# Performance work log

Measured on AMD Instinct MI355X. Metric: run time of the kernel, lower is better.

The kernel has to match this reference:

```python
import jax, jax.numpy as jnp
import numpy as np

# subgraph partition for subgraph_num == 7 (sums to 78 nodes)
GRAPH_LIST = [5, 9, 9, 25, 9, 9, 12]
EMB_SIZE = 30
PROJ_DIM = 10


def setup_inputs() -> dict:
    key = jax.random.key(0)
    k_x, k_c, k_w = jax.random.split(key, 3)
    B, N = 32768, sum(GRAPH_LIST)  # N = 78
    x = jax.random.normal(k_x, (B, N, EMB_SIZE), dtype=jnp.float32)
    coordinates = jax.random.normal(k_c, (N, 3), dtype=jnp.float32)
    stdv = 1.0 / np.sqrt(62.0)  # matches reset_parameters (trainable_vec size 62)
    weight = jax.random.uniform(k_w, (EMB_SIZE, PROJ_DIM), dtype=jnp.float32,
                                minval=-stdv, maxval=stdv)
    return {"x": x, "coordinates": coordinates, "weight": weight}


def reference(x, coordinates, weight):
    # x: [B, 78, 30] (already in subgraph-transformed order), coordinates: [78, 3]
    coarsen_feats, coarsen_coords = [], []
    idx = 0
    for length in GRAPH_LIST:  # static 7-way loop over fixed subgraph sizes
        sub_f = x[:, idx:idx + length]          # [B, j, 30]
        sub_c = coordinates[idx:idx + length]   # [j, 3]
        fw = jnp.einsum('bjg,gh->bjh', sub_f, weight)          # [B, j, 10]
        # sum_i (fw[b,j,:] . fw[b,i,:]) == fw[b,j,:] . sum_i fw[b,i,:]
        att_logits = jnp.einsum('bjh,bh->bj', fw, fw.sum(axis=1))  # [B, j]
        att = jax.nn.softmax(att_logits, axis=1)                   # [B, j]
        feat = jnp.einsum('bj,bjg->bg', att, sub_f)                # [B, 30]
        coor = jnp.mean(att @ sub_c, axis=0)                       # [3]
        coarsen_feats.append(feat[:, None, :])
        coarsen_coords.append(coor[None, :])
        idx += length
    coarsen_features = jnp.concatenate(coarsen_feats, axis=1)       # [B, 7, 30]
    coarsen_coordinates = jnp.concatenate(coarsen_coords, axis=0)   # [7, 3]
    return coarsen_features, coarsen_coordinates
```

## Files before the change

kernel.cpp:

```cpp
#include <hip/hip_runtime.h>
#include <math.h>

#define BTOT   32768
#define NNODE  78
#define NEMB   30
#define NPROJ  10
#define NGR    7
#define ROW    (NNODE*NEMB)
#define BPW    8
#define FEAT_OUT (BTOT*NGR*NEMB)
#define NSLOT  64
#define SLOTP  80

__constant__ int d_off[NGR] = {0,5,14,23,48,57,66};
__constant__ int d_len[NGR] = {5,9,9,25,9,9,12};

template<int CTRL>
__device__ __forceinline__ float dpp_f(float x) {
  return __int_as_float(__builtin_amdgcn_update_dpp(0, __float_as_int(x), CTRL, 0xF, 0xF, true));
}
__device__ __forceinline__ float swz16(float x) {
  return __int_as_float(__builtin_amdgcn_ds_swizzle(__float_as_int(x), 0x401F));
}
__device__ __forceinline__ float hsum32(float x) {
  x += dpp_f<0xB1>(x);
  x += dpp_f<0x4E>(x);
  x += dpp_f<0x141>(x);
  x += dpp_f<0x140>(x);
  x += swz16(x);
  return x;
}

template<int OFF, int LEN, int G>
__device__ __forceinline__ void process_graph(
    const float* __restrict__ xrow, const float (&Wr)[NPROJ],
    float* __restrict__ arow, float* __restrict__ outb,
    int lane31, bool evalid, int e)
{
  float xr[LEN];
  float xsum = 0.f;
#pragma unroll
  for (int j = 0; j < LEN; ++j) {
    xr[j] = xrow[(OFF + j) * NEMB + e];
    xsum += xr[j];
  }
  float t[NPROJ];
#pragma unroll
  for (int h = 0; h < NPROJ; ++h) t[h] = hsum32(Wr[h] * xsum);
  float u = 0.f;
#pragma unroll
  for (int h = 0; h < NPROJ; ++h) u = fmaf(Wr[h], t[h], u);
  float lg[LEN];
#pragma unroll
  for (int j = 0; j < LEN; ++j) lg[j] = hsum32(xr[j] * u);
  float m = lg[0];
#pragma unroll
  for (int j = 1; j < LEN; ++j) m = fmaxf(m, lg[j]);
  float s = 0.f;
#pragma unroll
  for (int j = 0; j < LEN; ++j) { lg[j] = __expf(lg[j] - m); s += lg[j]; }
  float inv = 1.f / s;
  float f = 0.f, myatt = 0.f;
#pragma unroll
  for (int j = 0; j < LEN; ++j) {
    float a = lg[j] * inv;
    f = fmaf(a, xr[j], f);
    if (lane31 == j) myatt = a;
  }
  if (evalid) outb[G * NEMB + e] = f;
  if (lane31 < LEN) arow[OFF + lane31] = myatt;
}

__global__ __launch_bounds__(256) void meso_main(
    const float* __restrict__ x, const float* __restrict__ wt,
    float* __restrict__ out, float* __restrict__ attpart)
{
  __shared__ float att_all[BPW][NNODE];

  const int tid    = threadIdx.x;
  const int half   = tid >> 5;
  const int lane31 = tid & 31;
  const bool evalid = lane31 < NEMB;
  const int e = evalid ? lane31 : (NEMB - 1);

  float Wr[NPROJ];
#pragma unroll
  for (int h = 0; h < NPROJ; ++h) Wr[h] = evalid ? wt[e * NPROJ + h] : 0.f;

  const long long b = (long long)blockIdx.x * BPW + half;
  const float* xrow = x + b * ROW;
  float* outb = out + b * (NGR * NEMB);
  float* arow = att_all[half];

  process_graph< 0, 5,0>(xrow, Wr, arow, outb, lane31, evalid, e);
  process_graph< 5, 9,1>(xrow, Wr, arow, outb, lane31, evalid, e);
  process_graph<14, 9,2>(xrow, Wr, arow, outb, lane31, evalid, e);
  process_graph<23,25,3>(xrow, Wr, arow, outb, lane31, evalid, e);
  process_graph<48, 9,4>(xrow, Wr, arow, outb, lane31, evalid, e);
  process_graph<57, 9,5>(xrow, Wr, arow, outb, lane31, evalid, e);
  process_graph<66,12,6>(xrow, Wr, arow, outb, lane31, evalid, e);

  __syncthreads();
  if (tid < NNODE) {
    float s = 0.f;
#pragma unroll
    for (int h = 0; h < BPW; ++h) s += att_all[h][tid];
    atomicAdd(&attpart[(blockIdx.x & (NSLOT-1)) * SLOTP + tid], s);
  }
}

__global__ __launch_bounds__(128) void meso_coor(
    const float* __restrict__ attpart,
    const float* __restrict__ coords,
    float* __restrict__ out_coor)
{
  __shared__ float asum[NNODE];
  int t = threadIdx.x;
  if (t < NNODE) {
    float s = 0.f;
#pragma unroll
    for (int k = 0; k < NSLOT; ++k) s += attpart[k * SLOTP + t];
    asum[t] = s;
  }
  __syncthreads();
  if (t < NGR*3) {
    int g = t / 3, kk = t % 3;
    int off = d_off[g], len = d_len[g];
    float s = 0.f;
    for (int j = 0; j < len; ++j) s += asum[off+j] * coords[(off+j)*3 + kk];
    out_coor[t] = s * (1.0f/(float)BTOT);
  }
}

extern "C" void kernel_launch(void* const* d_in, const int* in_sizes, int n_in,
                              void* d_out, int out_size, void* d_ws, size_t ws_size,
                              hipStream_t stream) {
  const float* x      = (const float*)d_in[0];
  const float* coords = (const float*)d_in[1];
  const float* wt     = (const float*)d_in[2];
  float* out     = (float*)d_out;
  float* attpart = (float*)d_ws;

  hipMemsetAsync(attpart, 0, NSLOT * SLOTP * sizeof(float), stream);
  meso_main<<<BTOT/BPW, 256, 0, stream>>>(x, wt, out, attpart);
  meso_coor<<<1, 128, 0, stream>>>(attpart, coords, out + FEAT_OUT);
}
```

Baseline: 82.81 us.

## Split main kernel grid across subgraphs, one block per (batch tile, graph)

Each block now handles a single subgraph for its 8 batch rows instead of all seven, so the grid grows sevenfold and the blocks diverge by graph through a switch on blockIdx mod 7. The aim is more parallelism and shorter per-block dependency chains, giving more waves in flight to hide memory latency. In exchange the weight loads and per-block setup are repeated seven times, the work per block is uneven (5 to 25 nodes), and there are more atomics into the partial attention slots.

```diff
diff --git a/kernel.cpp b/kernel.cpp
--- a/kernel.cpp
+++ b/kernel.cpp
@@ -68,14 +68,18 @@
     if (lane31 == j) myatt = a;
   }
   if (evalid) outb[G * NEMB + e] = f;
-  if (lane31 < LEN) arow[OFF + lane31] = myatt;
+  if (lane31 < LEN) arow[lane31] = myatt;
 }
 
 __global__ __launch_bounds__(256) void meso_main(
     const float* __restrict__ x, const float* __restrict__ wt,
     float* __restrict__ out, float* __restrict__ attpart)
 {
-  __shared__ float att_all[BPW][NNODE];
+  __shared__ float att_all[BPW][32];
+
+  const int bid = blockIdx.x;
+  const int g   = bid % NGR;
+  const long long bb = bid / NGR;
 
   const int tid    = threadIdx.x;
   const int half   = tid >> 5;
@@ -87,25 +91,28 @@
 #pragma unroll
   for (int h = 0; h < NPROJ; ++h) Wr[h] = evalid ? wt[e * NPROJ + h] : 0.f;
 
-  const long long b = (long long)blockIdx.x * BPW + half;
+  const long long b = bb * BPW + half;
   const float* xrow = x + b * ROW;
   float* outb = out + b * (NGR * NEMB);
   float* arow = att_all[half];
 
-  process_graph< 0, 5,0>(xrow, Wr, arow, outb, lane31, evalid, e);
-  process_graph< 5, 9,1>(xrow, Wr, arow, outb, lane31, evalid, e);
-  process_graph<14, 9,2>(xrow, Wr, arow, outb, lane31, evalid, e);
-  process_graph<23,25,3>(xrow, Wr, arow, outb, lane31, evalid, e);
-  process_graph<48, 9,4>(xrow, Wr, arow, outb, lane31, evalid, e);
-  process_graph<57, 9,5>(xrow, Wr, arow, outb, lane31, evalid, e);
-  process_graph<66,12,6>(xrow, Wr, arow, outb, lane31, evalid, e);
+  switch (g) {
+    case 0: process_graph< 0, 5,0>(xrow, Wr, arow, outb, lane31, evalid, e); break;
+    case 1: process_graph< 5, 9,1>(xrow, Wr, arow, outb, lane31, evalid, e); break;
+    case 2: process_graph<14, 9,2>(xrow, Wr, arow, outb, lane31, evalid, e); break;
+    case 3: process_graph<23,25,3>(xrow, Wr, arow, outb, lane31, evalid, e); break;
+    case 4: process_graph<48, 9,4>(xrow, Wr, arow, outb, lane31, evalid, e); break;
+    case 5: process_graph<57, 9,5>(xrow, Wr, arow, outb, lane31, evalid, e); break;
+    case 6: process_graph<66,12,6>(xrow, Wr, arow, outb, lane31, evalid, e); break;
+  }
 
   __syncthreads();
-  if (tid < NNODE) {
+  const int off = d_off[g], len = d_len[g];
+  if (tid < len) {
     float s = 0.f;
 #pragma unroll
     for (int h = 0; h < BPW; ++h) s += att_all[h][tid];
-    atomicAdd(&attpart[(blockIdx.x & (NSLOT-1)) * SLOTP + tid], s);
+    atomicAdd(&attpart[((int)(bb & (NSLOT-1))) * SLOTP + off + tid], s);
   }
 }
 
@@ -142,6 +149,6 @@
   float* attpart = (float*)d_ws;
 
   hipMemsetAsync(attpart, 0, NSLOT * SLOTP * sizeof(float), stream);
-  meso_main<<<BTOT/BPW, 256, 0, stream>>>(x, wt, out, attpart);
+  meso_main<<<(BTOT/BPW)*NGR, 256, 0, stream>>>(x, wt, out, attpart);
   meso_coor<<<1, 128, 0, stream>>>(attpart, coords, out + FEAT_OUT);
 }
```

Result: slower. 96.13 us (+16.1%).

## Vectorize x loads as float2 pairs and drop atomics for per-block attention partials

Applied to the files above, without the earlier changes.

Each 32-lane half-wave now splits into two 16-lane groups that each handle alternate nodes, loading two embedding values per lane as float2. This cuts the reduction to 16-lane DPP plus one swizzle and moves the loads of the next subgraph ahead of the current subgraph's compute. The atomicAdd into 64 slots and the memset are replaced by plain per-block stores of attention sums. The coordinate kernel becomes 21 blocks that each reduce over all 4096 per-block partials. This removes atomic contention and a memset launch, but adds a larger partial buffer (about 1.3 MB) for the second kernel to read.

```diff
diff --git a/kernel.cpp b/kernel.cpp
--- a/kernel.cpp
+++ b/kernel.cpp
@@ -9,8 +9,8 @@
 #define ROW    (NNODE*NEMB)
 #define BPW    8
 #define FEAT_OUT (BTOT*NGR*NEMB)
-#define NSLOT  64
-#define SLOTP  80
+#define NWG    (BTOT/BPW)
+#define APITCH 80
 
 __constant__ int d_off[NGR] = {0,5,14,23,48,57,66};
 __constant__ int d_len[NGR] = {5,9,9,25,9,9,12};
@@ -22,53 +22,88 @@
 __device__ __forceinline__ float swz16(float x) {
   return __int_as_float(__builtin_amdgcn_ds_swizzle(__float_as_int(x), 0x401F));
 }
-__device__ __forceinline__ float hsum32(float x) {
+__device__ __forceinline__ float hsum16(float x) {
   x += dpp_f<0xB1>(x);
   x += dpp_f<0x4E>(x);
   x += dpp_f<0x141>(x);
   x += dpp_f<0x140>(x);
-  x += swz16(x);
   return x;
 }
 
+template<int NP>
+__device__ __forceinline__ void load_pairs(const float* __restrict__ base,
+                                           float2 (&xr)[NP]) {
+#pragma unroll
+  for (int p = 0; p < NP; ++p)
+    xr[p] = *(const float2*)(base + p * (2*NEMB));
+}
+
 template<int OFF, int LEN, int G>
-__device__ __forceinline__ void process_graph(
-    const float* __restrict__ xrow, const float (&Wr)[NPROJ],
+__device__ __forceinline__ void compute_graph(
+    const float2 (&xr)[(LEN+1)/2],
+    const float (&W0)[NPROJ], const float (&W1)[NPROJ],
     float* __restrict__ arow, float* __restrict__ outb,
-    int lane31, bool evalid, int e)
+    bool isB, int lmod)
 {
-  float xr[LEN];
-  float xsum = 0.f;
-#pragma unroll
-  for (int j = 0; j < LEN; ++j) {
-    xr[j] = xrow[(OFF + j) * NEMB + e];
-    xsum += xr[j];
-  }
+  constexpr int NP  = (LEN+1)/2;
+  constexpr int NB  = LEN/2;
+  constexpr bool ODD = (LEN & 1);
+
+  float xs0 = 0.f, xs1 = 0.f;
+#pragma unroll
+  for (int p = 0; p < NP; ++p) {
+    float mk = (ODD && p == NP-1) ? (isB ? 0.f : 1.f) : 1.f;
+    xs0 += mk * xr[p].x;
+    xs1 += mk * xr[p].y;
+  }
+  xs0 += swz16(xs0);
+  xs1 += swz16(xs1);
   float t[NPROJ];
 #pragma unroll
-  for (int h = 0; h < NPROJ; ++h) t[h] = hsum32(Wr[h] * xsum);
-  float u = 0.f;
-#pragma unroll
-  for (int h = 0; h < NPROJ; ++h) u = fmaf(Wr[h], t[h], u);
-  float lg[LEN];
-#pragma unroll
-  for (int j = 0; j < LEN; ++j) lg[j] = hsum32(xr[j] * u);
-  float m = lg[0];
-#pragma unroll
-  for (int j = 1; j < LEN; ++j) m = fmaxf(m, lg[j]);
-  float s = 0.f;
-#pragma unroll
-  for (int j = 0; j < LEN; ++j) { lg[j] = __expf(lg[j] - m); s += lg[j]; }
-  float inv = 1.f / s;
-  float f = 0.f, myatt = 0.f;
-#pragma unroll
-  for (int j = 0; j < LEN; ++j) {
-    float a = lg[j] * inv;
-    f = fmaf(a, xr[j], f);
-    if (lane31 == j) myatt = a;
-  }
-  if (evalid) outb[G * NEMB + e] = f;
-  if (lane31 < LEN) arow[OFF + lane31] = myatt;
+  for (int h = 0; h < NPROJ; ++h)
+    t[h] = hsum16(fmaf(W1[h], xs1, W0[h]*xs0));
+  float u0 = 0.f, u1 = 0.f;
+#pragma unroll
+  for (int h = 0; h < NPROJ; ++h) { u0 = fmaf(W0[h], t[h], u0); u1 = fmaf(W1[h], t[h], u1); }
+  float lg[NP];
+#pragma unroll
+  for (int p = 0; p < NP; ++p)
+    lg[p] = hsum16(fmaf(xr[p].y, u1, xr[p].x * u0));
+  float mp = -INFINITY;
+#pragma unroll
+  for (int p = 0; p < NP; ++p) {
+    float v = lg[p];
+    if (ODD && p == NP-1 && isB) v = -INFINITY;
+    mp = fmaxf(mp, v);
+  }
+  float m = fmaxf(mp, swz16(mp));
+  float ex[NP];
+  float sp = 0.f;
+#pragma unroll
+  for (int p = 0; p < NP; ++p) {
+    float v = __expf(lg[p] - m);
+    if (ODD && p == NP-1 && isB) v = 0.f;
+    ex[p] = v; sp += v;
+  }
+  float inv = 1.f / (sp + swz16(sp));
+  float f0 = 0.f, f1 = 0.f;
+#pragma unroll
+  for (int p = 0; p < NP; ++p) {
+    float a = ex[p] * inv;
+    f0 = fmaf(a, xr[p].x, f0);
+    f1 = fmaf(a, xr[p].y, f1);
+  }
+  f0 += swz16(f0);
+  f1 += swz16(f1);
+  if (!isB && lmod < 15)
+    *(float2*)(outb + G*NEMB + 2*lmod) = make_float2(f0, f1);
+  float myatt = 0.f; bool wr = false;
+#pragma unroll
+  for (int p = 0; p < NP; ++p) {
+    bool pick = isB ? (p < NB && lmod == p) : (lmod == p);
+    if (pick) { myatt = ex[p] * inv; wr = true; }
+  }
+  if (wr) arow[OFF + 2*lmod + (isB ? 1 : 0)] = myatt;
 }
 
 __global__ __launch_bounds__(256) void meso_main(
@@ -80,56 +115,75 @@
   const int tid    = threadIdx.x;
   const int half   = tid >> 5;
   const int lane31 = tid & 31;
-  const bool evalid = lane31 < NEMB;
-  const int e = evalid ? lane31 : (NEMB - 1);
-
-  float Wr[NPROJ];
-#pragma unroll
-  for (int h = 0; h < NPROJ; ++h) Wr[h] = evalid ? wt[e * NPROJ + h] : 0.f;
+  const bool isB   = lane31 >= 16;
+  const int lmod   = lane31 & 15;
+  const int lmodc  = lmod < 15 ? lmod : 14;
+  const bool wvalid = lmod < 15;
+
+  float W0[NPROJ], W1[NPROJ];
+#pragma unroll
+  for (int h = 0; h < NPROJ; ++h) {
+    W0[h] = wvalid ? wt[(2*lmod  )*NPROJ + h] : 0.f;
+    W1[h] = wvalid ? wt[(2*lmod+1)*NPROJ + h] : 0.f;
+  }
 
   const long long b = (long long)blockIdx.x * BPW + half;
-  const float* xrow = x + b * ROW;
-  float* outb = out + b * (NGR * NEMB);
+  const float* xbase = x + b*ROW + (isB ? NEMB : 0) + 2*lmodc;
+  float* outb = out + b * (NGR*NEMB);
   float* arow = att_all[half];
 
-  process_graph< 0, 5,0>(xrow, Wr, arow, outb, lane31, evalid, e);
-  process_graph< 5, 9,1>(xrow, Wr, arow, outb, lane31, evalid, e);
-  process_graph<14, 9,2>(xrow, Wr, arow, outb, lane31, evalid, e);
-  process_graph<23,25,3>(xrow, Wr, arow, outb, lane31, evalid, e);
-  process_graph<48, 9,4>(xrow, Wr, arow, outb, lane31, evalid, e);
-  process_graph<57, 9,5>(xrow, Wr, arow, outb, lane31, evalid, e);
-  process_graph<66,12,6>(xrow, Wr, arow, outb, lane31, evalid, e);
+  float2 xr0[3], xr1[5], xr2[5], xr3[13], xr4[5], xr5[5], xr6[6];
+  load_pairs< 3>(xbase +  0*NEMB, xr0);
+  load_pairs< 5>(xbase +  5*NEMB, xr1);
+  compute_graph< 0, 5,0>(xr0, W0,W1, arow, outb, isB, lmod);
+  load_pairs< 5>(xbase + 14*NEMB, xr2);
+  compute_graph< 5, 9,1>(xr1, W0,W1, arow, outb, isB, lmod);
+  load_pairs<13>(xbase + 23*NEMB, xr3);
+  compute_graph<14, 9,2>(xr2, W0,W1, arow, outb, isB, lmod);
+  load_pairs< 5>(xbase + 48*NEMB, xr4);
+  compute_graph<23,25,3>(xr3, W0,W1, arow, outb, isB, lmod);
+  load_pairs< 5>(xbase + 57*NEMB, xr5);
+  compute_graph<48, 9,4>(xr4, W0,W1, arow, outb, isB, lmod);
+  load_pairs< 6>(xbase + 66*NEMB, xr6);
+  compute_graph<57, 9,5>(xr5, W0,W1, arow, outb, isB, lmod);
+  compute_graph<66,12,6>(xr6, W0,W1, arow, outb, isB, lmod);
 
   __syncthreads();
   if (tid < NNODE) {
     float s = 0.f;
 #pragma unroll
     for (int h = 0; h < BPW; ++h) s += att_all[h][tid];
-    atomicAdd(&attpart[(blockIdx.x & (NSLOT-1)) * SLOTP + tid], s);
-  }
-}
-
-__global__ __launch_bounds__(128) void meso_coor(
+    attpart[(size_t)blockIdx.x * APITCH + tid] = s;
+  }
+}
+
+__global__ __launch_bounds__(256) void meso_coor(
     const float* __restrict__ attpart,
     const float* __restrict__ coords,
     float* __restrict__ out_coor)
 {
-  __shared__ float asum[NNODE];
-  int t = threadIdx.x;
-  if (t < NNODE) {
+  __shared__ float red[256];
+  const int t  = blockIdx.x;
+  const int g  = t / 3, kk = t % 3;
+  const int off = d_off[g], len = d_len[g];
+  const int tid = threadIdx.x;
+
+  float partial = 0.f;
+  for (int j = 0; j < len; ++j) {
+    float c = coords[(off+j)*3 + kk];
     float s = 0.f;
-#pragma unroll
-    for (int k = 0; k < NSLOT; ++k) s += attpart[k * SLOTP + t];
-    asum[t] = s;
-  }
+    for (int w = tid; w < NWG; w += 256)
+      s += attpart[(size_t)w * APITCH + off + j];
+    partial = fmaf(c, s, partial);
+  }
+  red[tid] = partial;
   __syncthreads();
-  if (t < NGR*3) {
-    int g = t / 3, kk = t % 3;
-    int off = d_off[g], len = d_len[g];
-    float s = 0.f;
-    for (int j = 0; j < len; ++j) s += asum[off+j] * coords[(off+j)*3 + kk];
-    out_coor[t] = s * (1.0f/(float)BTOT);
-  }
+#pragma unroll
+  for (int k = 128; k > 0; k >>= 1) {
+    if (tid < k) red[tid] += red[tid + k];
+    __syncthreads();
+  }
+  if (tid == 0) out_coor[t] = red[0] * (1.0f/(float)BTOT);
 }
 
 extern "C" void kernel_launch(void* const* d_in, const int* in_sizes, int n_in,
@@ -141,7 +195,6 @@
   float* out     = (float*)d_out;
   float* attpart = (float*)d_ws;
 
-  hipMemsetAsync(attpart, 0, NSLOT * SLOTP * sizeof(float), stream);
-  meso_main<<<BTOT/BPW, 256, 0, stream>>>(x, wt, out, attpart);
-  meso_coor<<<1, 128, 0, stream>>>(attpart, coords, out + FEAT_OUT);
-}
+  meso_main<<<NWG, 256, 0, stream>>>(x, wt, out, attpart);
+  meso_coor<<<21, 256, 0, stream>>>(attpart, coords, out + FEAT_OUT);
+}
```

After: 137.1 us. 65.5% more time.
